# Kernel optimization log

Hardware: AMD Instinct MI355X
Metric: run time of the kernel (lower is better)

## Reference

```python
import jax, jax.numpy as jnp
import numpy as np

H = 3.0        # args.h smoothing length
N_NODES = 100000
DIM_HIDDEN = 128
D = 3


def setup_inputs() -> dict:
    key = jax.random.key(0)
    ks = jax.random.split(key, 10)
    E = 1600000
    v = jax.random.normal(ks[0], (N_NODES, D), dtype=jnp.float32)
    r_ij = jax.random.normal(ks[1], (E, D), dtype=jnp.float32)
    edge_index = jax.random.randint(ks[2], (2, E), 0, N_NODES, dtype=jnp.int64)
    # teacher MLP params: [1+D] -> dim_hidden -> dim_hidden -> 1
    def lin(k, fan_in, fan_out):
        bound = 1.0 / np.sqrt(fan_in)
        kw, kb = jax.random.split(k)
        W = jax.random.uniform(kw, (fan_out, fan_in), jnp.float32, -bound, bound)
        b = jax.random.uniform(kb, (fan_out,), jnp.float32, -bound, bound)
        return W, b
    W0, b0 = lin(ks[3], 1 + D, DIM_HIDDEN)
    W1, b1 = lin(ks[4], DIM_HIDDEN, DIM_HIDDEN)
    W2, b2 = lin(ks[5], DIM_HIDDEN, 1)
    return {"v": v, "r_ij": r_ij, "W0": W0, "b0": b0, "W1": W1, "b1": b1,
            "W2": W2, "b2": b2, "edge_index": edge_index}


def _teacher(x, W0, b0, W1, b1, W2, b2):
    x = jax.nn.silu(x @ W0.T + b0)
    x = jax.nn.silu(x @ W1.T + b1)
    return x @ W2.T + b2  # [E, 1]


def _scatter_mean(x, idx, n):
    s = jax.ops.segment_sum(x, idx, num_segments=n)
    c = jax.ops.segment_sum(jnp.ones((idx.shape[0], 1), x.dtype), idx, num_segments=n)
    return s / jnp.maximum(c, 1.0)


def reference(v, r_ij, W0, b0, W1, b1, W2, b2, edge_index):
    i = edge_index[0]
    j = edge_index[1]
    v_ij = v[i] - v[j]                                   # [E, D] gather-diff
    r_ = jnp.sqrt(jnp.sum(r_ij * r_ij, axis=-1, keepdims=True)) / H  # [E, 1]
    m_i = _teacher(jnp.concatenate([r_, v_ij], axis=-1), W0, b0, W1, b1, W2, b2)
    m_j = _teacher(jnp.concatenate([r_, -v_ij], axis=-1), W0, b0, W1, b1, W2, b2)
    S = _scatter_mean(m_i, i, N_NODES) + _scatter_mean(m_j, j, N_NODES)  # [N, 1]
    return S
```

## Files before the change

### kernel.cpp

```cpp
#include <hip/hip_runtime.h>

typedef unsigned short ushort_t;
typedef __bf16 bf16x8 __attribute__((ext_vector_type(8)));
typedef __bf16 bf16x2 __attribute__((ext_vector_type(2)));
typedef float f32x4 __attribute__((ext_vector_type(4)));

__device__ __forceinline__ ushort_t f2bf(float f) {
    unsigned u;
    __builtin_memcpy(&u, &f, 4);
    u += 0x7fffu + ((u >> 16) & 1u);
    return (ushort_t)(u >> 16);
}

__device__ __forceinline__ float silu(float x) {
    float e = __builtin_amdgcn_exp2f(x * -1.442695040888963f);
    return x * __builtin_amdgcn_rcpf(1.0f + e);
}

__device__ __forceinline__ float rdlane(float v, int l) {
    return __builtin_bit_cast(float, __builtin_amdgcn_readlane(__builtin_bit_cast(int, v), l));
}


__global__ __launch_bounds__(256, 2) void mlp_kernel(
    const float* __restrict__ v,
    const float* __restrict__ rij,
    const float* __restrict__ W0,
    const float* __restrict__ b0,
    const float* __restrict__ W1,
    const float* __restrict__ b1,
    const float* __restrict__ W2,
    const float* __restrict__ b2,
    const int* __restrict__ eidx,
    float* __restrict__ sum_i, float* __restrict__ sum_j,
    unsigned* __restrict__ cnt_i, unsigned* __restrict__ cnt_j,
    int E, int nchunks)
{
    __shared__ ushort_t sW1[16384];
    __shared__ ushort_t sH0[16384];

    const int tid  = threadIdx.x;
    const int lane = tid & 63;
    const int wave = tid >> 6;

    {
        int n = tid >> 1, half = tid & 1;
        const float* src = W1 + n * 128;
#pragma unroll
        for (int dk = 0; dk < 8; dk++) {
            int k0   = half * 64 + dk * 8;
            int frag = (n >> 4) * 4 + (k0 >> 5);
            int slot = (n & 15) + 16 * ((k0 >> 3) & 3);
            ushort_t tmp[8];
#pragma unroll
            for (int t = 0; t < 8; t++) tmp[t] = f2bf(src[k0 + t]);
            *(uint4*)(&sW1[frag * 512 + slot * 8]) = *(const uint4*)tmp;
        }
    }

    float4 w0q[2]; float b0v[2];
#pragma unroll
    for (int kk = 0; kk < 2; kk++) {
        int h = 2 * lane + kk;
        w0q[kk].x = W0[h * 4 + 0];
        w0q[kk].y = W0[h * 4 + 1];
        w0q[kk].z = W0[h * 4 + 2];
        w0q[kk].w = W0[h * 4 + 3];
        b0v[kk]   = b0[h];
    }
    float b1v[8], w2v[8];
#pragma unroll
    for (int nt = 0; nt < 8; nt++) {
        int ccol = nt * 16 + (lane & 15);
        b1v[nt] = b1[ccol];
        w2v[nt] = W2[ccol];
    }
    const float b2f = b2[0];

    __syncthreads();

    const int q = lane >> 4, c = lane & 15, p = (lane >> 2) & 3, bsub = lane & 3;

    for (int chunk = blockIdx.x; chunk < nchunks; chunk += gridDim.x) {
        const int ebase = chunk * 64 + wave * 16;

        const int ple  = lane >> 2;
        const int comp = lane & 3;
        const int pe   = ebase + ple;
        float val = 0.f;
        int idx_reg = 0;
        if (pe < E) {
            if (comp == 3) {
                float r0 = rij[3 * pe], r1 = rij[3 * pe + 1], r2 = rij[3 * pe + 2];
                val = sqrtf(fmaf(r0, r0, fmaf(r1, r1, r2 * r2))) * (1.0f / 3.0f);
            } else {
                int i = eidx[pe], j = eidx[E + pe];
                idx_reg = (comp == 1) ? j : i;
                val = v[3 * i + comp] - v[3 * j + comp];
                if (comp == 0) atomicAdd(&cnt_i[i], 1u);
                if (comp == 1) atomicAdd(&cnt_j[j], 1u);
            }
        }

#pragma unroll
        for (int le = 0; le < 16; le++) {
            float vx = rdlane(val, le * 4 + 0);
            float vy = rdlane(val, le * 4 + 1);
            float vz = rdlane(val, le * 4 + 2);
            float rr = rdlane(val, le * 4 + 3);
            float si[2], sj[2];
#pragma unroll
            for (int kk = 0; kk < 2; kk++) {
                float cc = fmaf(w0q[kk].x, rr, b0v[kk]);
                float dd = fmaf(w0q[kk].y, vx, fmaf(w0q[kk].z, vy, w0q[kk].w * vz));
                si[kk] = silu(cc + dd);
                sj[kk] = silu(cc - dd);
            }
            bf16x2 pki, pkj;
            pki[0] = (__bf16)si[0]; pki[1] = (__bf16)si[1];
            pkj[0] = (__bf16)sj[0]; pkj[1] = (__bf16)sj[1];
            int mi = wave * 32 + 2 * le;
            int fr_i = ((mi >> 4) << 2) + q;
            int fr_j = (((mi + 1) >> 4) << 2) + q;
            int sl_i = (((mi & 15) ^ q ^ (p << 2)) & 15) + (p << 4);
            int sl_j = ((((mi + 1) & 15) ^ q ^ (p << 2)) & 15) + (p << 4);
            ((unsigned*)sH0)[fr_i * 256 + sl_i * 4 + bsub] = __builtin_bit_cast(unsigned, pki);
            ((unsigned*)sH0)[fr_j * 256 + sl_j * 4 + bsub] = __builtin_bit_cast(unsigned, pkj);
        }

        f32x4 acc[2][8];
#pragma unroll
        for (int t = 0; t < 2; t++)
#pragma unroll
            for (int nt = 0; nt < 8; nt++)
                acc[t][nt] = (f32x4){0.f, 0.f, 0.f, 0.f};

#pragma unroll
        for (int ks = 0; ks < 4; ks++) {
            int sl_rd = (((lane & 15) ^ ks ^ (q << 2)) & 15) + 16 * q;
            bf16x8 a0 = *(const bf16x8*)(&sH0[((2 * wave + 0) * 4 + ks) * 512 + sl_rd * 8]);
            bf16x8 a1 = *(const bf16x8*)(&sH0[((2 * wave + 1) * 4 + ks) * 512 + sl_rd * 8]);
#pragma unroll
            for (int nt = 0; nt < 8; nt++) {
                bf16x8 bb = *(const bf16x8*)(&sW1[(nt * 4 + ks) * 512 + lane * 8]);
                acc[0][nt] = __builtin_amdgcn_mfma_f32_16x16x32_bf16(a0, bb, acc[0][nt], 0, 0, 0);
                acc[1][nt] = __builtin_amdgcn_mfma_f32_16x16x32_bf16(a1, bb, acc[1][nt], 0, 0, 0);
            }
        }

        float rs[2][4] = {{0.f, 0.f, 0.f, 0.f}, {0.f, 0.f, 0.f, 0.f}};
#pragma unroll
        for (int t = 0; t < 2; t++)
#pragma unroll
            for (int nt = 0; nt < 8; nt++)
#pragma unroll
                for (int r = 0; r < 4; r++) {
                    float x = acc[t][nt][r] + b1v[nt];
                    rs[t][r] = fmaf(silu(x), w2v[nt], rs[t][r]);
                }
#pragma unroll
        for (int t = 0; t < 2; t++)
#pragma unroll
            for (int r = 0; r < 4; r++) {
                float s = rs[t][r];
                s += __shfl_xor(s, 1, 64);
                s += __shfl_xor(s, 2, 64);
                s += __shfl_xor(s, 4, 64);
                s += __shfl_xor(s, 8, 64);
                int el  = t * 8 + q * 2 + (r >> 1);
                int src = el * 4 + (r & 1);
                int node = __shfl(idx_reg, src, 64);
                int e = ebase + el;
                if (c == 0 && e < E) {
                    if (r & 1) atomicAdd(&sum_j[node], s + b2f);
                    else       atomicAdd(&sum_i[node], s + b2f);
                }
            }
    }
}

__global__ void finalize_kernel(const float* __restrict__ sum_i, const float* __restrict__ sum_j,
                                const unsigned* __restrict__ cnt_i, const unsigned* __restrict__ cnt_j,
                                float* __restrict__ out, int N)
{
    int n = blockIdx.x * 256 + threadIdx.x;
    if (n < N) {
        float a = sum_i[n] / fmaxf((float)cnt_i[n], 1.0f);
        float bsum = sum_j[n] / fmaxf((float)cnt_j[n], 1.0f);
        out[n] = a + bsum;
    }
}

extern "C" void kernel_launch(void* const* d_in, const int* in_sizes, int n_in,
                              void* d_out, int out_size, void* d_ws, size_t ws_size,
                              hipStream_t stream) {
    const float* v   = (const float*)d_in[0];
    const float* rij = (const float*)d_in[1];
    const float* W0  = (const float*)d_in[2];
    const float* b0  = (const float*)d_in[3];
    const float* W1  = (const float*)d_in[4];
    const float* b1  = (const float*)d_in[5];
    const float* W2  = (const float*)d_in[6];
    const float* b2  = (const float*)d_in[7];
    const int* eidx  = (const int*)d_in[8];

    const int E = in_sizes[1] / 3;
    const int N = out_size;

    float* sum_i = (float*)d_ws;
    float* sum_j = sum_i + N;
    unsigned* cnt_i = (unsigned*)(sum_j + N);
    unsigned* cnt_j = cnt_i + N;

    hipMemsetAsync(d_ws, 0, (size_t)4 * N * sizeof(float), stream);

    int nchunks = (E + 63) / 64;
    int grid = nchunks < 512 ? nchunks : 512;
    mlp_kernel<<<grid, 256, 0, stream>>>(v, rij, W0, b0, W1, b1, W2, b2, eidx,
                                         sum_i, sum_j, cnt_i, cnt_j, E, nchunks);
    finalize_kernel<<<(N + 255) / 256, 256, 0, stream>>>(sum_i, sum_j, cnt_i, cnt_j,
                                                         (float*)d_out, N);
}
```

Measured before the change: 438.7 us.

## Pack count into fp64 atomic sum and prefetch next chunk's edge data

Replaces the separate float sum and unsigned count atomics with a single fp64 atomicAdd per endpoint. Each add carries the value plus a fixed offset of 65536, and the finalize kernel recovers the count and the sum by rounding. This halves the number of scattered atomics and removes the count arrays. It also software-pipelines the gather of edge indices, v and r_ij for the next chunk behind the current chunk's MLP compute. The costs are more registers, fp64 atomics, and precision or aliasing risk if a node's sum magnitude nears the count unit.

Measured after the change: 424.8 us. 3.2% less time.

```diff
diff --git a/kernel.cpp b/kernel.cpp
--- a/kernel.cpp
+++ b/kernel.cpp
@@ -21,6 +21,8 @@
     return __builtin_bit_cast(float, __builtin_amdgcn_readlane(__builtin_bit_cast(int, v), l));
 }
 
+
+#define CNT_UNIT 65536.0
 
 __global__ __launch_bounds__(256, 2) void mlp_kernel(
     const float* __restrict__ v,
@@ -32,8 +34,7 @@
     const float* __restrict__ W2,
     const float* __restrict__ b2,
     const int* __restrict__ eidx,
-    float* __restrict__ sum_i, float* __restrict__ sum_j,
-    unsigned* __restrict__ cnt_i, unsigned* __restrict__ cnt_j,
+    double* __restrict__ acc_i, double* __restrict__ acc_j,
     int E, int nchunks)
 {
     __shared__ ushort_t sW1[16384];
@@ -80,34 +81,41 @@
     __syncthreads();
 
     const int q = lane >> 4, c = lane & 15, p = (lane >> 2) & 3, bsub = lane & 3;
-
-    for (int chunk = blockIdx.x; chunk < nchunks; chunk += gridDim.x) {
-        const int ebase = chunk * 64 + wave * 16;
-
-        const int ple  = lane >> 2;
-        const int comp = lane & 3;
-        const int pe   = ebase + ple;
-        float val = 0.f;
-        int idx_reg = 0;
-        if (pe < E) {
+    const int ple  = lane >> 2;
+    const int comp = lane & 3;
+
+    auto preload = [&](int ch, float& val_o, int& idx_o) {
+        float val = 0.f; int idxr = 0;
+        int pe = ch * 64 + wave * 16 + ple;
+        if (ch < nchunks && pe < E) {
             if (comp == 3) {
                 float r0 = rij[3 * pe], r1 = rij[3 * pe + 1], r2 = rij[3 * pe + 2];
                 val = sqrtf(fmaf(r0, r0, fmaf(r1, r1, r2 * r2))) * (1.0f / 3.0f);
             } else {
-                int i = eidx[pe], j = eidx[E + pe];
-                idx_reg = (comp == 1) ? j : i;
-                val = v[3 * i + comp] - v[3 * j + comp];
-                if (comp == 0) atomicAdd(&cnt_i[i], 1u);
-                if (comp == 1) atomicAdd(&cnt_j[j], 1u);
-            }
-        }
+                int i = eidx[pe], jj = eidx[E + pe];
+                idxr = (comp == 1) ? jj : i;
+                val = v[3 * i + comp] - v[3 * jj + comp];
+            }
+        }
+        val_o = val; idx_o = idxr;
+    };
+
+    float val; int idxr;
+    preload(blockIdx.x, val, idxr);
+
+    for (int chunk = blockIdx.x; chunk < nchunks; chunk += gridDim.x) {
+        const float val_cur = val;
+        const int   idx_cur = idxr;
+        preload(chunk + (int)gridDim.x, val, idxr);
+
+        const int ebase = chunk * 64 + wave * 16;
 
 #pragma unroll
         for (int le = 0; le < 16; le++) {
-            float vx = rdlane(val, le * 4 + 0);
-            float vy = rdlane(val, le * 4 + 1);
-            float vz = rdlane(val, le * 4 + 2);
-            float rr = rdlane(val, le * 4 + 3);
+            float vx = rdlane(val_cur, le * 4 + 0);
+            float vy = rdlane(val_cur, le * 4 + 1);
+            float vz = rdlane(val_cur, le * 4 + 2);
+            float rr = rdlane(val_cur, le * 4 + 3);
             float si[2], sj[2];
 #pragma unroll
             for (int kk = 0; kk < 2; kk++) {
@@ -169,25 +177,29 @@
                 s += __shfl_xor(s, 8, 64);
                 int el  = t * 8 + q * 2 + (r >> 1);
                 int src = el * 4 + (r & 1);
-                int node = __shfl(idx_reg, src, 64);
+                int node = __shfl(idx_cur, src, 64);
                 int e = ebase + el;
                 if (c == 0 && e < E) {
-                    if (r & 1) atomicAdd(&sum_j[node], s + b2f);
-                    else       atomicAdd(&sum_i[node], s + b2f);
+                    double contrib = (double)(s + b2f) + CNT_UNIT;
+                    if (r & 1) atomicAdd(&acc_j[node], contrib);
+                    else       atomicAdd(&acc_i[node], contrib);
                 }
             }
     }
 }
 
-__global__ void finalize_kernel(const float* __restrict__ sum_i, const float* __restrict__ sum_j,
-                                const unsigned* __restrict__ cnt_i, const unsigned* __restrict__ cnt_j,
+__global__ void finalize_kernel(const double* __restrict__ acc_i,
+                                const double* __restrict__ acc_j,
                                 float* __restrict__ out, int N)
 {
     int n = blockIdx.x * 256 + threadIdx.x;
     if (n < N) {
-        float a = sum_i[n] / fmaxf((float)cnt_i[n], 1.0f);
-        float bsum = sum_j[n] / fmaxf((float)cnt_j[n], 1.0f);
-        out[n] = a + bsum;
+        double ti = acc_i[n], tj = acc_j[n];
+        double ci = rint(ti * (1.0 / CNT_UNIT));
+        double cj = rint(tj * (1.0 / CNT_UNIT));
+        double si = ti - ci * CNT_UNIT;
+        double sj = tj - cj * CNT_UNIT;
+        out[n] = (float)(si / fmax(ci, 1.0) + sj / fmax(cj, 1.0));
     }
 }
 
@@ -207,17 +219,15 @@
     const int E = in_sizes[1] / 3;
     const int N = out_size;
 
-    float* sum_i = (float*)d_ws;
-    float* sum_j = sum_i + N;
-    unsigned* cnt_i = (unsigned*)(sum_j + N);
-    unsigned* cnt_j = cnt_i + N;
-
-    hipMemsetAsync(d_ws, 0, (size_t)4 * N * sizeof(float), stream);
+    double* acc_i = (double*)d_ws;
+    double* acc_j = acc_i + N;
+
+    hipMemsetAsync(d_ws, 0, (size_t)2 * N * sizeof(double), stream);
 
     int nchunks = (E + 63) / 64;
     int grid = nchunks < 512 ? nchunks : 512;
     mlp_kernel<<<grid, 256, 0, stream>>>(v, rij, W0, b0, W1, b1, W2, b2, eidx,
-                                         sum_i, sum_j, cnt_i, cnt_j, E, nchunks);
-    finalize_kernel<<<(N + 255) / 256, 256, 0, stream>>>(sum_i, sum_j, cnt_i, cnt_j,
+                                         acc_i, acc_j, E, nchunks);
+    finalize_kernel<<<(N + 255) / 256, 256, 0, stream>>>(acc_i, acc_j,
                                                          (float*)d_out, N);
 }
```
